# Kernel tuning notes

Hardware: AMD Instinct MI355X
Metric: run time of the kernel (lower is better)

## Reference

```python
import jax, jax.numpy as jnp
import numpy as np

CHEBY_K = 3

def _normalize_adj(A):
    # A: [B, N, N]
    A = jnp.maximum(A, 0.0)
    N = A.shape[-1]
    A = A + jnp.eye(N, dtype=A.dtype)[None, :, :]
    D = jnp.maximum(A.sum(-1), 1e-6)          # [B, N]
    D_inv_sqrt = D ** -0.5
    return D_inv_sqrt[..., :, None] * A * D_inv_sqrt[..., None, :]


def setup_inputs() -> dict:
    key = jax.random.key(0)
    k1, k2, k3, k4, k5 = jax.random.split(key, 5)
    B, N, F_in, F_out, E = 16, 512, 64, 64, 16
    x = jax.random.normal(k1, (B, N, F_in), dtype=jnp.float32)
    emb = jax.random.normal(k2, (B, N, E), dtype=jnp.float32)
    A = jax.random.uniform(k3, (B, N, N), dtype=jnp.float32)
    # xavier-uniform-like init for pools
    lim_w = float(np.sqrt(6.0 / (E * CHEBY_K * F_in + F_out)))
    weights_pool = jax.random.uniform(k4, (E, CHEBY_K, F_in, F_out), dtype=jnp.float32,
                                      minval=-lim_w, maxval=lim_w)
    lim_b = float(np.sqrt(6.0 / (E + F_out)))
    bias_pool = jax.random.uniform(k5, (E, F_out), dtype=jnp.float32,
                                   minval=-lim_b, maxval=lim_b)
    return {"x": x, "emb": emb, "A": A,
            "weights_pool": weights_pool, "bias_pool": bias_pool}


def reference(x, emb, A, weights_pool, bias_pool):
    B, N, F_in = x.shape
    K = CHEBY_K
    A_hat = _normalize_adj(A)                                   # [B,N,N]
    t0 = jnp.broadcast_to(jnp.eye(N, dtype=x.dtype)[None], (B, N, N))
    supports = [t0, A_hat]
    for _ in range(2, K):
        supports.append(2.0 * jnp.matmul(A_hat, supports[-1]) - supports[-2])
    supports = jnp.stack(supports, axis=1)                      # [B,K,N,N]
    x_g = jnp.einsum('bknm,bmf->bknf', supports, x)             # [B,K,N,F_in]
    # fused per-node adaptive conv: avoids materializing [B,K,N,F_in,F_out]
    out = jnp.einsum('bknf,bne,ekfo->bno', x_g, emb, weights_pool)
    out = out + jnp.einsum('bne,eo->bno', emb, bias_pool)       # [B,N,F_out]
    return out
```

## Files before the change

kernel.cpp:

```cpp
#include <hip/hip_runtime.h>
#include <hip/hip_bf16.h>

#define NB 16
#define NN 512
#define NF 64
#define NE 16
#define NKF 192
#define NNODE (NB*NN)

typedef __hip_bfloat16 bf16;
typedef __attribute__((ext_vector_type(8))) short short8;
typedef __attribute__((ext_vector_type(4))) float f32x4;

typedef const __attribute__((address_space(1))) char gchar;
typedef __attribute__((address_space(3))) char lchar;

__device__ inline void gload16(const void* g, void* l) {
    __builtin_amdgcn_global_load_lds((gchar*)g, (lchar*)l, 16, 0, 0);
}

__device__ inline short f2bs(float f) {
    union { bf16 b; short s; } u; u.b = __float2bfloat16(f); return u.s;
}

__global__ __launch_bounds__(256) void k_pre(
    const float* __restrict__ A, const float* __restrict__ x,
    const float* __restrict__ Wp, float* __restrict__ dis,
    bf16* __restrict__ xg, bf16* __restrict__ xT, bf16* __restrict__ Bt) {
    __shared__ float Ts[64][66];
    int bid = blockIdx.x, tid = threadIdx.x;
    if (bid < 2048) {
        int row = bid * 4 + (tid >> 6);
        int lane = tid & 63;
        const float* a = A + (size_t)row * NN;
        float s = 0.f;
        #pragma unroll
        for (int j = 0; j < NN / 64; ++j) s += fmaxf(a[lane + 64 * j], 0.f);
        #pragma unroll
        for (int off = 32; off >= 1; off >>= 1) s += __shfl_down(s, off, 64);
        if (lane == 0) dis[row] = rsqrtf(fmaxf(s + 1.0f, 1e-6f));
    } else if (bid < 2176) {
        int node0 = (bid - 2048) * 64;
        int r = tid >> 2, f0 = (tid & 3) * 16;
        const float* xp = x + (size_t)(node0 + r) * NF + f0;
        float v[16];
        #pragma unroll
        for (int i = 0; i < 16; ++i) v[i] = xp[i];
        short8 p0, p1;
        #pragma unroll
        for (int i = 0; i < 8; ++i) { p0[i] = f2bs(v[i]); p1[i] = f2bs(v[8 + i]); }
        *(short8*)&xg[(size_t)(node0 + r) * NKF + f0] = p0;
        *(short8*)&xg[(size_t)(node0 + r) * NKF + f0 + 8] = p1;
        #pragma unroll
        for (int i = 0; i < 4; ++i)
            *(float4*)&Ts[r][f0 + i * 4] = *(const float4*)(v + i * 4);
        __syncthreads();
        int f = tid >> 2, nq0 = (tid & 3) * 16;
        int b = node0 >> 9, nloc = node0 & (NN - 1);
        bf16* xt = xT + (size_t)(b * NF + f) * NN + nloc + nq0;
        #pragma unroll
        for (int h = 0; h < 2; ++h) {
            short8 o;
            #pragma unroll
            for (int i = 0; i < 8; ++i) o[i] = f2bs(Ts[nq0 + h * 8 + i][f]);
            *(short8*)&xt[h * 8] = o;
        }
    } else {
        int q = bid - 2176;
        int e = q / 3, kt = q % 3;
        int r = tid >> 2, o0 = (tid & 3) * 16;
        const float* wp = Wp + (size_t)e * (NKF * NF) + (size_t)(kt * 64 + r) * NF + o0;
        #pragma unroll
        for (int i = 0; i < 4; ++i)
            *(float4*)&Ts[r][o0 + i * 4] = *(const float4*)(wp + i * 4);
        __syncthreads();
        int o = tid >> 2, r0 = (tid & 3) * 16;
        bf16* bt = Bt + (size_t)(e * 64 + o) * NKF + kt * 64 + r0;
        #pragma unroll
        for (int h = 0; h < 2; ++h) {
            short8 w;
            #pragma unroll
            for (int i = 0; i < 8; ++i) w[i] = f2bs(Ts[r0 + h * 8 + i][o]);
            *(short8*)&bt[h * 8] = w;
        }
    }
}

__global__ __launch_bounds__(256) void k_ahat(
    const float* __restrict__ A, const float* __restrict__ dis,
    bf16* __restrict__ Ah) {
    int tid = threadIdx.x;
    int row = blockIdx.x * 4 + (tid >> 6);
    int m0 = (tid & 63) * 8;
    int b = row >> 9, n = row & (NN - 1);
    const float* db = dis + b * NN;
    float dn = db[n];
    const float* ap = A + (size_t)row * NN + m0;
    float4 a0 = *(const float4*)ap, a1 = *(const float4*)(ap + 4);
    float4 d0 = *(const float4*)(db + m0), d1 = *(const float4*)(db + m0 + 4);
    float av[8] = {a0.x, a0.y, a0.z, a0.w, a1.x, a1.y, a1.z, a1.w};
    float dm[8] = {d0.x, d0.y, d0.z, d0.w, d1.x, d1.y, d1.z, d1.w};
    short8 o;
    #pragma unroll
    for (int i = 0; i < 8; ++i) {
        float v = fmaxf(av[i], 0.f) + ((n == m0 + i) ? 1.f : 0.f);
        o[i] = f2bs(v * dn * dm[i]);
    }
    *(short8*)&Ah[(size_t)row * NN + m0] = o;
}

template <int PASS>
__global__ __launch_bounds__(256) void k_spmm(
    const short* __restrict__ Ah, const short* __restrict__ Bsrc,
    const float* __restrict__ x, bf16* __restrict__ xg, bf16* __restrict__ y1T) {
    __shared__ short As[64 * 32];
    __shared__ short Xs[64 * 32];
    __shared__ float Cs[64][66];
    int tid = threadIdx.x, lane = tid & 63, w = tid >> 6;
    int n0 = blockIdx.x * 64, b = blockIdx.y;
    const short* Ab = Ah + (size_t)b * NN * NN;
    const short* Xb = Bsrc + (size_t)b * NF * NN;

    int sr = tid >> 2;
    int p  = tid & 3;
    int cA = p ^ ((sr >> 1) & 3);

    int fr = lane & 15;
    int fc = ((lane >> 4) ^ ((fr >> 1) & 3)) * 8;

    f32x4 acc[4] = {};

    for (int kt = 0; kt < 16; ++kt) {
        __syncthreads();
        gload16(Ab + (size_t)(n0 + sr) * NN + kt * 32 + cA * 8, As + tid * 8);
        gload16(Xb + (size_t)sr * NN + kt * 32 + cA * 8, Xs + tid * 8);
        __syncthreads();
        short8 afr = *(const short8*)&As[(16 * w + fr) * 32 + fc];
        #pragma unroll
        for (int j = 0; j < 4; ++j) {
            short8 bfr = *(const short8*)&Xs[(16 * j + fr) * 32 + fc];
            acc[j] = __builtin_amdgcn_mfma_f32_16x16x32_bf16(afr, bfr, acc[j], 0, 0, 0);
        }
    }

    #pragma unroll
    for (int j = 0; j < 4; ++j)
        #pragma unroll
        for (int r = 0; r < 4; ++r)
            Cs[16 * w + 4 * (lane >> 4) + r][16 * j + (lane & 15)] = acc[j][r];
    __syncthreads();

    int nl = tid >> 2, f0 = (tid & 3) * 16;
    size_t node = (size_t)b * NN + n0 + nl;
    float cv[16];
    #pragma unroll
    for (int i = 0; i < 16; ++i) cv[i] = Cs[nl][f0 + i];
    if (PASS == 0) {
        short8 p0, p1;
        #pragma unroll
        for (int i = 0; i < 8; ++i) { p0[i] = f2bs(cv[i]); p1[i] = f2bs(cv[8 + i]); }
        *(short8*)&xg[node * NKF + 64 + f0] = p0;
        *(short8*)&xg[node * NKF + 64 + f0 + 8] = p1;
        int f = tid >> 2, nq0 = (tid & 3) * 16;
        bf16* yt = y1T + (size_t)(b * NF + f) * NN + n0 + nq0;
        #pragma unroll
        for (int h = 0; h < 2; ++h) {
            short8 o;
            #pragma unroll
            for (int i = 0; i < 8; ++i) o[i] = f2bs(Cs[nq0 + h * 8 + i][f]);
            *(short8*)&yt[h * 8] = o;
        }
    } else {
        const float* xp = x + node * NF + f0;
        short8 p0, p1;
        #pragma unroll
        for (int i = 0; i < 8; ++i) {
            p0[i] = f2bs(2.f * cv[i] - xp[i]);
            p1[i] = f2bs(2.f * cv[8 + i] - xp[8 + i]);
        }
        *(short8*)&xg[node * NKF + 128 + f0] = p0;
        *(short8*)&xg[node * NKF + 128 + f0 + 8] = p1;
    }
}

__global__ __launch_bounds__(256) void k_fused(
    const short* __restrict__ xg, const short* __restrict__ Bt,
    const float* __restrict__ emb, const float* __restrict__ bpool,
    float* __restrict__ out) {
    __shared__ short Axs[32 * 192];
    __shared__ short Bts[2][64 * 192];
    int tid = threadIdx.x, lane = tid & 63, w = tid >> 6;
    int node0 = blockIdx.x * 32;

    {
        int kk0 = tid >> 7;
        int r = (tid >> 2) & 31;
        int slot = tid & 3;
        int cA = slot ^ ((r >> 1) & 3);
        #pragma unroll
        for (int h = 0; h < 3; ++h) {
            int kk = h * 2 + kk0;
            gload16(xg + (size_t)(node0 + r) * NKF + kk * 32 + cA * 8,
                    Axs + h * 2048 + tid * 8);
        }
    }
    int br = tid >> 2, bslot = tid & 3;
    int bcA = bslot ^ ((br >> 1) & 3);
    #pragma unroll
    for (int kk = 0; kk < 6; ++kk)
        gload16(Bt + (size_t)(0 * 64 + br) * NKF + kk * 32 + bcA * 8,
                Bts[0] + kk * 2048 + br * 32 + bslot * 8);
    __syncthreads();

    int fr = lane & 15, ak = lane >> 4;
    int arow = 16 * (w & 1) + fr;
    short8 afr[6];
    #pragma unroll
    for (int kk = 0; kk < 6; ++kk)
        afr[kk] = *(const short8*)&Axs[kk * 1024 + arow * 32 + ((ak ^ ((arow >> 1) & 3)) * 8)];

    float oacc[2][4] = {};
    int cur = 0;
    for (int e = 0; e < NE; ++e) {
        if (e < NE - 1) {
            #pragma unroll
            for (int kk = 0; kk < 6; ++kk)
                gload16(Bt + (size_t)((e + 1) * 64 + br) * NKF + kk * 32 + bcA * 8,
                        Bts[cur ^ 1] + kk * 2048 + br * 32 + bslot * 8);
        }
        f32x4 acc[2] = {};
        #pragma unroll
        for (int j = 0; j < 2; ++j) {
            int brow = 32 * (w >> 1) + 16 * j + fr;
            #pragma unroll
            for (int kk = 0; kk < 6; ++kk) {
                short8 bfr = *(const short8*)&Bts[cur][kk * 2048 + brow * 32 +
                                                       ((ak ^ ((brow >> 1) & 3)) * 8)];
                acc[j] = __builtin_amdgcn_mfma_f32_16x16x32_bf16(afr[kk], bfr, acc[j], 0, 0, 0);
            }
        }
        #pragma unroll
        for (int j = 0; j < 2; ++j) {
            int col = 32 * (w >> 1) + 16 * j + fr;
            float bv = bpool[e * NF + col];
            #pragma unroll
            for (int r = 0; r < 4; ++r) {
                int nl = 16 * (w & 1) + ak * 4 + r;
                float ev = emb[(size_t)(node0 + nl) * NE + e];
                oacc[j][r] = fmaf(ev, acc[j][r] + bv, oacc[j][r]);
            }
        }
        __syncthreads();
        cur ^= 1;
    }

    #pragma unroll
    for (int j = 0; j < 2; ++j) {
        int col = 32 * (w >> 1) + 16 * j + fr;
        #pragma unroll
        for (int r = 0; r < 4; ++r) {
            int nl = 16 * (w & 1) + ak * 4 + r;
            out[(size_t)(node0 + nl) * NF + col] = oacc[j][r];
        }
    }
}

extern "C" void kernel_launch(void* const* d_in, const int* in_sizes, int n_in,
                              void* d_out, int out_size, void* d_ws, size_t ws_size,
                              hipStream_t stream) {
    const float* x   = (const float*)d_in[0];
    const float* emb = (const float*)d_in[1];
    const float* A   = (const float*)d_in[2];
    const float* Wp  = (const float*)d_in[3];
    const float* bp  = (const float*)d_in[4];
    float* out = (float*)d_out;

    float* ws  = (float*)d_ws;
    float* dis = ws;
    bf16*  xT  = (bf16*)(ws + 8192);
    bf16*  y1T = (bf16*)(ws + 270336);
    bf16*  xg  = (bf16*)(ws + 532480);
    bf16*  Bt  = (bf16*)(ws + 1318912);
    bf16*  Ah  = (bf16*)(ws + 1417216);

    k_pre<<<2224, 256, 0, stream>>>(A, x, Wp, dis, xg, xT, Bt);
    k_ahat<<<2048, 256, 0, stream>>>(A, dis, Ah);
    dim3 g2(NN / 64, NB);
    k_spmm<0><<<g2, 256, 0, stream>>>((const short*)Ah, (const short*)xT, x, xg, y1T);
    k_spmm<1><<<g2, 256, 0, stream>>>((const short*)Ah, (const short*)y1T, x, xg, y1T);
    k_fused<<<NNODE / 32, 256, 0, stream>>>((const short*)xg, (const short*)Bt, emb, bp, out);
}
```

Baseline: 48.39 us.

## Fuse all stages into one persistent kernel with grid-wide atomic barriers

Replaces the five separate launches (degree, A-hat, two SpMM passes, fused output GEMM) with one persistent kernel of 256 blocks that loops over work units per stage and synchronizes the stages with atomic-counter grid barriers. The counters are cleared with a memset before the launch. It also stages each tile's emb values in shared memory rather than reading them from global memory inside the inner loop. This is meant to remove per-launch overhead and the gaps between kernels. The cost is fewer blocks in flight for the memory-bound stages, the spin-wait time at each barrier, and a risk of deadlock if the blocks are not all resident at once.

```diff
diff --git a/kernel.cpp b/kernel.cpp
--- a/kernel.cpp
+++ b/kernel.cpp
@@ -23,102 +23,29 @@
     union { bf16 b; short s; } u; u.b = __float2bfloat16(f); return u.s;
 }
 
-__global__ __launch_bounds__(256) void k_pre(
-    const float* __restrict__ A, const float* __restrict__ x,
-    const float* __restrict__ Wp, float* __restrict__ dis,
-    bf16* __restrict__ xg, bf16* __restrict__ xT, bf16* __restrict__ Bt) {
-    __shared__ float Ts[64][66];
-    int bid = blockIdx.x, tid = threadIdx.x;
-    if (bid < 2048) {
-        int row = bid * 4 + (tid >> 6);
-        int lane = tid & 63;
-        const float* a = A + (size_t)row * NN;
-        float s = 0.f;
-        #pragma unroll
-        for (int j = 0; j < NN / 64; ++j) s += fmaxf(a[lane + 64 * j], 0.f);
-        #pragma unroll
-        for (int off = 32; off >= 1; off >>= 1) s += __shfl_down(s, off, 64);
-        if (lane == 0) dis[row] = rsqrtf(fmaxf(s + 1.0f, 1e-6f));
-    } else if (bid < 2176) {
-        int node0 = (bid - 2048) * 64;
-        int r = tid >> 2, f0 = (tid & 3) * 16;
-        const float* xp = x + (size_t)(node0 + r) * NF + f0;
-        float v[16];
-        #pragma unroll
-        for (int i = 0; i < 16; ++i) v[i] = xp[i];
-        short8 p0, p1;
-        #pragma unroll
-        for (int i = 0; i < 8; ++i) { p0[i] = f2bs(v[i]); p1[i] = f2bs(v[8 + i]); }
-        *(short8*)&xg[(size_t)(node0 + r) * NKF + f0] = p0;
-        *(short8*)&xg[(size_t)(node0 + r) * NKF + f0 + 8] = p1;
-        #pragma unroll
-        for (int i = 0; i < 4; ++i)
-            *(float4*)&Ts[r][f0 + i * 4] = *(const float4*)(v + i * 4);
-        __syncthreads();
-        int f = tid >> 2, nq0 = (tid & 3) * 16;
-        int b = node0 >> 9, nloc = node0 & (NN - 1);
-        bf16* xt = xT + (size_t)(b * NF + f) * NN + nloc + nq0;
-        #pragma unroll
-        for (int h = 0; h < 2; ++h) {
-            short8 o;
-            #pragma unroll
-            for (int i = 0; i < 8; ++i) o[i] = f2bs(Ts[nq0 + h * 8 + i][f]);
-            *(short8*)&xt[h * 8] = o;
-        }
-    } else {
-        int q = bid - 2176;
-        int e = q / 3, kt = q % 3;
-        int r = tid >> 2, o0 = (tid & 3) * 16;
-        const float* wp = Wp + (size_t)e * (NKF * NF) + (size_t)(kt * 64 + r) * NF + o0;
-        #pragma unroll
-        for (int i = 0; i < 4; ++i)
-            *(float4*)&Ts[r][o0 + i * 4] = *(const float4*)(wp + i * 4);
-        __syncthreads();
-        int o = tid >> 2, r0 = (tid & 3) * 16;
-        bf16* bt = Bt + (size_t)(e * 64 + o) * NKF + kt * 64 + r0;
-        #pragma unroll
-        for (int h = 0; h < 2; ++h) {
-            short8 w;
-            #pragma unroll
-            for (int i = 0; i < 8; ++i) w[i] = f2bs(Ts[r0 + h * 8 + i][o]);
-            *(short8*)&bt[h * 8] = w;
-        }
-    }
-}
-
-__global__ __launch_bounds__(256) void k_ahat(
-    const float* __restrict__ A, const float* __restrict__ dis,
-    bf16* __restrict__ Ah) {
-    int tid = threadIdx.x;
-    int row = blockIdx.x * 4 + (tid >> 6);
-    int m0 = (tid & 63) * 8;
-    int b = row >> 9, n = row & (NN - 1);
-    const float* db = dis + b * NN;
-    float dn = db[n];
-    const float* ap = A + (size_t)row * NN + m0;
-    float4 a0 = *(const float4*)ap, a1 = *(const float4*)(ap + 4);
-    float4 d0 = *(const float4*)(db + m0), d1 = *(const float4*)(db + m0 + 4);
-    float av[8] = {a0.x, a0.y, a0.z, a0.w, a1.x, a1.y, a1.z, a1.w};
-    float dm[8] = {d0.x, d0.y, d0.z, d0.w, d1.x, d1.y, d1.z, d1.w};
-    short8 o;
-    #pragma unroll
-    for (int i = 0; i < 8; ++i) {
-        float v = fmaxf(av[i], 0.f) + ((n == m0 + i) ? 1.f : 0.f);
-        o[i] = f2bs(v * dn * dm[i]);
-    }
-    *(short8*)&Ah[(size_t)row * NN + m0] = o;
+__device__ __forceinline__ void gbar(unsigned* cnt, int nb) {
+    __syncthreads();
+    if (threadIdx.x == 0) {
+        __threadfence();
+        __hip_atomic_fetch_add(cnt, 1u, __ATOMIC_RELEASE, __HIP_MEMORY_SCOPE_AGENT);
+        while (__hip_atomic_load(cnt, __ATOMIC_ACQUIRE, __HIP_MEMORY_SCOPE_AGENT)
+               < (unsigned)nb)
+            __builtin_amdgcn_s_sleep(1);
+        __threadfence();
+    }
+    __syncthreads();
 }
 
 template <int PASS>
-__global__ __launch_bounds__(256) void k_spmm(
-    const short* __restrict__ Ah, const short* __restrict__ Bsrc,
-    const float* __restrict__ x, bf16* __restrict__ xg, bf16* __restrict__ y1T) {
-    __shared__ short As[64 * 32];
-    __shared__ short Xs[64 * 32];
-    __shared__ float Cs[64][66];
-    int tid = threadIdx.x, lane = tid & 63, w = tid >> 6;
-    int n0 = blockIdx.x * 64, b = blockIdx.y;
-    const short* Ab = Ah + (size_t)b * NN * NN;
+__device__ __forceinline__ void spmm_unit(
+    char* smem, int tid, int lane, int w, int n0, int b,
+    const short* __restrict__ AhS, const short* __restrict__ Bsrc,
+    const float* __restrict__ x, bf16* __restrict__ xg, bf16* __restrict__ y1T)
+{
+    short* As = (short*)smem;
+    short* Xs = (short*)(smem + 4096);
+    float (*Cs)[66] = (float (*)[66])(smem + 8192);
+    const short* Ab = AhS + (size_t)b * NN * NN;
     const short* Xb = Bsrc + (size_t)b * NF * NN;
 
     int sr = tid >> 2;
@@ -181,86 +108,192 @@
         *(short8*)&xg[node * NKF + 128 + f0] = p0;
         *(short8*)&xg[node * NKF + 128 + f0 + 8] = p1;
     }
-}
-
-__global__ __launch_bounds__(256) void k_fused(
-    const short* __restrict__ xg, const short* __restrict__ Bt,
-    const float* __restrict__ emb, const float* __restrict__ bpool,
-    float* __restrict__ out) {
-    __shared__ short Axs[32 * 192];
-    __shared__ short Bts[2][64 * 192];
+    __syncthreads();
+}
+
+__global__ __launch_bounds__(256) void k_mega(
+    const float* __restrict__ A, const float* __restrict__ x,
+    const float* __restrict__ Wp, const float* __restrict__ emb,
+    const float* __restrict__ bpool, float* __restrict__ dis,
+    bf16* __restrict__ xg, bf16* __restrict__ xT, bf16* __restrict__ y1T,
+    bf16* __restrict__ Bt, bf16* __restrict__ Ah, float* __restrict__ out,
+    unsigned* __restrict__ cnt)
+{
+    __shared__ __attribute__((aligned(16))) char smem[63488];
     int tid = threadIdx.x, lane = tid & 63, w = tid >> 6;
-    int node0 = blockIdx.x * 32;
+    int nb = gridDim.x;
+
+    for (int g = blockIdx.x; g < 2048; g += nb) {
+        int row = g * 4 + w;
+        const float* a = A + (size_t)row * NN;
+        float s = 0.f;
+        #pragma unroll
+        for (int j = 0; j < NN / 64; ++j) s += fmaxf(a[lane + 64 * j], 0.f);
+        #pragma unroll
+        for (int off = 32; off >= 1; off >>= 1) s += __shfl_down(s, off, 64);
+        if (lane == 0) dis[row] = rsqrtf(fmaxf(s + 1.0f, 1e-6f));
+    }
+    gbar(cnt + 0, nb);
 
     {
-        int kk0 = tid >> 7;
-        int r = (tid >> 2) & 31;
-        int slot = tid & 3;
-        int cA = slot ^ ((r >> 1) & 3);
-        #pragma unroll
-        for (int h = 0; h < 3; ++h) {
-            int kk = h * 2 + kk0;
-            gload16(xg + (size_t)(node0 + r) * NKF + kk * 32 + cA * 8,
-                    Axs + h * 2048 + tid * 8);
-        }
-    }
-    int br = tid >> 2, bslot = tid & 3;
-    int bcA = bslot ^ ((br >> 1) & 3);
-    #pragma unroll
-    for (int kk = 0; kk < 6; ++kk)
-        gload16(Bt + (size_t)(0 * 64 + br) * NKF + kk * 32 + bcA * 8,
-                Bts[0] + kk * 2048 + br * 32 + bslot * 8);
-    __syncthreads();
-
-    int fr = lane & 15, ak = lane >> 4;
-    int arow = 16 * (w & 1) + fr;
-    short8 afr[6];
-    #pragma unroll
-    for (int kk = 0; kk < 6; ++kk)
-        afr[kk] = *(const short8*)&Axs[kk * 1024 + arow * 32 + ((ak ^ ((arow >> 1) & 3)) * 8)];
-
-    float oacc[2][4] = {};
-    int cur = 0;
-    for (int e = 0; e < NE; ++e) {
-        if (e < NE - 1) {
+        float (*Ts)[66] = (float (*)[66])smem;
+        for (int u = blockIdx.x; u < 2224; u += nb) {
+            if (u < 2048) {
+                int row = u * 4 + w;
+                int m0 = lane * 8;
+                int b = row >> 9, n = row & (NN - 1);
+                const float* db = dis + b * NN;
+                float dn = db[n];
+                const float* ap = A + (size_t)row * NN + m0;
+                float4 a0 = *(const float4*)ap, a1 = *(const float4*)(ap + 4);
+                float4 d0 = *(const float4*)(db + m0), d1 = *(const float4*)(db + m0 + 4);
+                float av[8] = {a0.x, a0.y, a0.z, a0.w, a1.x, a1.y, a1.z, a1.w};
+                float dm[8] = {d0.x, d0.y, d0.z, d0.w, d1.x, d1.y, d1.z, d1.w};
+                short8 o;
+                #pragma unroll
+                for (int i = 0; i < 8; ++i) {
+                    float v = fmaxf(av[i], 0.f) + ((n == m0 + i) ? 1.f : 0.f);
+                    o[i] = f2bs(v * dn * dm[i]);
+                }
+                *(short8*)&Ah[(size_t)row * NN + m0] = o;
+            } else if (u < 2176) {
+                int node0 = (u - 2048) * 64;
+                int r = tid >> 2, f0 = (tid & 3) * 16;
+                const float* xp = x + (size_t)(node0 + r) * NF + f0;
+                float v[16];
+                #pragma unroll
+                for (int i = 0; i < 16; ++i) v[i] = xp[i];
+                short8 p0, p1;
+                #pragma unroll
+                for (int i = 0; i < 8; ++i) { p0[i] = f2bs(v[i]); p1[i] = f2bs(v[8 + i]); }
+                *(short8*)&xg[(size_t)(node0 + r) * NKF + f0] = p0;
+                *(short8*)&xg[(size_t)(node0 + r) * NKF + f0 + 8] = p1;
+                #pragma unroll
+                for (int i = 0; i < 4; ++i)
+                    *(float4*)&Ts[r][f0 + i * 4] = *(const float4*)(v + i * 4);
+                __syncthreads();
+                int f = tid >> 2, nq0 = (tid & 3) * 16;
+                int b = node0 >> 9, nloc = node0 & (NN - 1);
+                bf16* xt = xT + (size_t)(b * NF + f) * NN + nloc + nq0;
+                #pragma unroll
+                for (int h = 0; h < 2; ++h) {
+                    short8 o;
+                    #pragma unroll
+                    for (int i = 0; i < 8; ++i) o[i] = f2bs(Ts[nq0 + h * 8 + i][f]);
+                    *(short8*)&xt[h * 8] = o;
+                }
+                __syncthreads();
+            } else {
+                int q = u - 2176;
+                int e = q / 3, kt = q % 3;
+                int r = tid >> 2, o0 = (tid & 3) * 16;
+                const float* wp = Wp + (size_t)e * (NKF * NF) + (size_t)(kt * 64 + r) * NF + o0;
+                #pragma unroll
+                for (int i = 0; i < 4; ++i)
+                    *(float4*)&Ts[r][o0 + i * 4] = *(const float4*)(wp + i * 4);
+                __syncthreads();
+                int o = tid >> 2, r0 = (tid & 3) * 16;
+                bf16* bt = Bt + (size_t)(e * 64 + o) * NKF + kt * 64 + r0;
+                #pragma unroll
+                for (int h = 0; h < 2; ++h) {
+                    short8 wv;
+                    #pragma unroll
+                    for (int i = 0; i < 8; ++i) wv[i] = f2bs(Ts[r0 + h * 8 + i][o]);
+                    *(short8*)&bt[h * 8] = wv;
+                }
+                __syncthreads();
+            }
+        }
+    }
+    gbar(cnt + 1, nb);
+
+    for (int u = blockIdx.x; u < 128; u += nb)
+        spmm_unit<0>(smem, tid, lane, w, (u & 7) * 64, u >> 3,
+                     (const short*)Ah, (const short*)xT, x, xg, y1T);
+    gbar(cnt + 2, nb);
+
+    for (int u = blockIdx.x; u < 128; u += nb)
+        spmm_unit<1>(smem, tid, lane, w, (u & 7) * 64, u >> 3,
+                     (const short*)Ah, (const short*)y1T, x, xg, y1T);
+    gbar(cnt + 3, nb);
+
+    {
+        short* Axs = (short*)smem;
+        short (*Bts)[12288] = (short (*)[12288])(smem + 12288);
+        float* Es = (float*)(smem + 61440);
+        for (int u = blockIdx.x; u < 256; u += nb) {
+            int node0 = u * 32;
+            {
+                int kk0 = tid >> 7;
+                int r = (tid >> 2) & 31;
+                int slot = tid & 3;
+                int cA = slot ^ ((r >> 1) & 3);
+                #pragma unroll
+                for (int h = 0; h < 3; ++h)
+                    gload16(xg + (size_t)(node0 + r) * NKF + (h * 2 + kk0) * 32 + cA * 8,
+                            Axs + h * 2048 + tid * 8);
+            }
+            int br = tid >> 2, bslot = tid & 3;
+            int bcA = bslot ^ ((br >> 1) & 3);
             #pragma unroll
             for (int kk = 0; kk < 6; ++kk)
-                gload16(Bt + (size_t)((e + 1) * 64 + br) * NKF + kk * 32 + bcA * 8,
-                        Bts[cur ^ 1] + kk * 2048 + br * 32 + bslot * 8);
-        }
-        f32x4 acc[2] = {};
-        #pragma unroll
-        for (int j = 0; j < 2; ++j) {
-            int brow = 32 * (w >> 1) + 16 * j + fr;
+                gload16(Bt + (size_t)br * NKF + kk * 32 + bcA * 8,
+                        (short*)Bts[0] + kk * 2048 + br * 32 + bslot * 8);
+            ((float2*)Es)[tid] = ((const float2*)(emb + (size_t)node0 * NE))[tid];
+            __syncthreads();
+
+            int fr = lane & 15, ak = lane >> 4;
+            int arow = 16 * (w & 1) + fr;
+            short8 afr[6];
             #pragma unroll
-            for (int kk = 0; kk < 6; ++kk) {
-                short8 bfr = *(const short8*)&Bts[cur][kk * 2048 + brow * 32 +
-                                                       ((ak ^ ((brow >> 1) & 3)) * 8)];
-                acc[j] = __builtin_amdgcn_mfma_f32_16x16x32_bf16(afr[kk], bfr, acc[j], 0, 0, 0);
+            for (int kk = 0; kk < 6; ++kk)
+                afr[kk] = *(const short8*)&Axs[kk * 1024 + arow * 32 +
+                                               ((ak ^ ((arow >> 1) & 3)) * 8)];
+
+            float oacc[2][4] = {};
+            int cur = 0;
+            for (int e = 0; e < NE; ++e) {
+                if (e < NE - 1) {
+                    #pragma unroll
+                    for (int kk = 0; kk < 6; ++kk)
+                        gload16(Bt + (size_t)((e + 1) * 64 + br) * NKF + kk * 32 + bcA * 8,
+                                (short*)Bts[cur ^ 1] + kk * 2048 + br * 32 + bslot * 8);
+                }
+                f32x4 acc[2] = {};
+                #pragma unroll
+                for (int j = 0; j < 2; ++j) {
+                    int brow = 32 * (w >> 1) + 16 * j + fr;
+                    #pragma unroll
+                    for (int kk = 0; kk < 6; ++kk) {
+                        short8 bfr = *(const short8*)&Bts[cur][kk * 2048 + brow * 32 +
+                                                              ((ak ^ ((brow >> 1) & 3)) * 8)];
+                        acc[j] = __builtin_amdgcn_mfma_f32_16x16x32_bf16(afr[kk], bfr, acc[j], 0, 0, 0);
+                    }
+                }
+                #pragma unroll
+                for (int j = 0; j < 2; ++j) {
+                    int col = 32 * (w >> 1) + 16 * j + fr;
+                    float bv = bpool[e * NF + col];
+                    #pragma unroll
+                    for (int r = 0; r < 4; ++r) {
+                        int nl = 16 * (w & 1) + ak * 4 + r;
+                        float ev = Es[nl * NE + e];
+                        oacc[j][r] = fmaf(ev, acc[j][r] + bv, oacc[j][r]);
+                    }
+                }
+                __syncthreads();
+                cur ^= 1;
             }
-        }
-        #pragma unroll
-        for (int j = 0; j < 2; ++j) {
-            int col = 32 * (w >> 1) + 16 * j + fr;
-            float bv = bpool[e * NF + col];
+
             #pragma unroll
-            for (int r = 0; r < 4; ++r) {
-                int nl = 16 * (w & 1) + ak * 4 + r;
-                float ev = emb[(size_t)(node0 + nl) * NE + e];
-                oacc[j][r] = fmaf(ev, acc[j][r] + bv, oacc[j][r]);
+            for (int j = 0; j < 2; ++j) {
+                int col = 32 * (w >> 1) + 16 * j + fr;
+                #pragma unroll
+                for (int r = 0; r < 4; ++r) {
+                    int nl = 16 * (w & 1) + ak * 4 + r;
+                    out[(size_t)(node0 + nl) * NF + col] = oacc[j][r];
+                }
             }
-        }
-        __syncthreads();
-        cur ^= 1;
-    }
-
-    #pragma unroll
-    for (int j = 0; j < 2; ++j) {
-        int col = 32 * (w >> 1) + 16 * j + fr;
-        #pragma unroll
-        for (int r = 0; r < 4; ++r) {
-            int nl = 16 * (w & 1) + ak * 4 + r;
-            out[(size_t)(node0 + nl) * NF + col] = oacc[j][r];
         }
     }
 }
@@ -268,11 +301,11 @@
 extern "C" void kernel_launch(void* const* d_in, const int* in_sizes, int n_in,
                               void* d_out, int out_size, void* d_ws, size_t ws_size,
                               hipStream_t stream) {
-    const float* x   = (const float*)d_in[0];
-    const float* emb = (const float*)d_in[1];
-    const float* A   = (const float*)d_in[2];
-    const float* Wp  = (const float*)d_in[3];
-    const float* bp  = (const float*)d_in[4];
+    const float* x    = (const float*)d_in[0];
+    const float* emb  = (const float*)d_in[1];
+    const float* Aad  = (const float*)d_in[2];
+    const float* Wp   = (const float*)d_in[3];
+    const float* bp   = (const float*)d_in[4];
     float* out = (float*)d_out;
 
     float* ws  = (float*)d_ws;
@@ -282,11 +315,9 @@
     bf16*  xg  = (bf16*)(ws + 532480);
     bf16*  Bt  = (bf16*)(ws + 1318912);
     bf16*  Ah  = (bf16*)(ws + 1417216);
-
-    k_pre<<<2224, 256, 0, stream>>>(A, x, Wp, dis, xg, xT, Bt);
-    k_ahat<<<2048, 256, 0, stream>>>(A, dis, Ah);
-    dim3 g2(NN / 64, NB);
-    k_spmm<0><<<g2, 256, 0, stream>>>((const short*)Ah, (const short*)xT, x, xg, y1T);
-    k_spmm<1><<<g2, 256, 0, stream>>>((const short*)Ah, (const short*)y1T, x, xg, y1T);
-    k_fused<<<NNODE / 32, 256, 0, stream>>>((const short*)xg, (const short*)Bt, emb, bp, out);
-}
+    unsigned* cnt = (unsigned*)(ws + 3514368);
+
+    hipMemsetAsync((void*)cnt, 0, 4 * sizeof(unsigned), stream);
+    k_mega<<<256, 256, 0, stream>>>(Aad, x, Wp, emb, bp, dis,
+                                    xg, xT, y1T, Bt, Ah, out, cnt);
+}
```

Measured after the change: 172.3 us. 256% more time.
